# Kernel tuning notes

Hardware: AMD Instinct MI355X
Metric: run time of the kernel (lower is better)

Reference implementation:

```python
import jax, jax.numpy as jnp
import numpy as np

D_MODEL = 1024
N_HEADS = 16
TOP_FACTOR = 5


def setup_inputs() -> dict:
    key = jax.random.key(0)
    ks = jax.random.split(key, 9)
    B, L, D = 2, 4096, D_MODEL
    s = 0.02
    return {
        "x": jax.random.normal(ks[0], (B, L, D), dtype=jnp.float32),
        "Wq": jax.random.normal(ks[1], (D, D), dtype=jnp.float32) * s,
        "bq": jnp.zeros((D,), dtype=jnp.float32),
        "Wk": jax.random.normal(ks[2], (D, D), dtype=jnp.float32) * s,
        "bk": jnp.zeros((D,), dtype=jnp.float32),
        "Wv": jax.random.normal(ks[3], (D, D), dtype=jnp.float32) * s,
        "bv": jnp.zeros((D,), dtype=jnp.float32),
        "Wo": jax.random.normal(ks[4], (D, D), dtype=jnp.float32) * s,
        "bo": jnp.zeros((D,), dtype=jnp.float32),
    }


def reference(x, Wq, bq, Wk, bk, Wv, bv, Wo, bo):
    B, L, D = x.shape
    H = N_HEADS
    hd = D // H
    BH = B * H
    top_u = max(1, L // TOP_FACTOR)

    def proj(W, b):
        # [B,L,D] -> [B*H, L, hd] (matches view + transpose(1,2) in torch)
        y = x @ W.T + b
        return y.reshape(B, L, H, hd).transpose(0, 2, 1, 3).reshape(BH, L, hd)

    Q = proj(Wq, bq)
    K = proj(Wk, bk)
    V = proj(Wv, bv)

    # select top-u queries per (batch,head) by L2 norm
    query_norms = jnp.linalg.norm(Q, axis=2)              # [BH, L]
    _, top_idx = jax.lax.top_k(query_norms, top_u)        # [BH, top_u]
    Q_sel = jnp.take_along_axis(Q, top_idx[:, :, None], axis=1)  # [BH, u, hd]

    scale = 1.0 / (hd ** 0.5)
    scores = jnp.einsum('bud,bld->bul', Q_sel, K) * scale  # [BH, u, L]
    attn = jax.nn.softmax(scores, axis=-1)
    out_sel = jnp.einsum('bul,bld->bud', attn, V)          # [BH, u, hd]

    # scatter selected outputs back; non-selected rows stay zero
    out_full = jnp.zeros((BH, L, hd), dtype=x.dtype)
    out_full = out_full.at[jnp.arange(BH)[:, None], top_idx].set(out_sel)

    out = out_full.reshape(B, H, L, hd).transpose(0, 2, 1, 3).reshape(B, L, D)
    return out @ Wo.T + bo
```

## Files before the change

### kernel.cpp

```cpp
#include <hip/hip_runtime.h>
#include <cstddef>
#include <cstdint>

constexpr int LSEQ = 4096;
constexpr int DM   = 1024;
constexpr int HD   = 64;
constexpr int BHT  = 32;
constexpr int TOPU = 819;
constexpr int MROWS = 8192;

typedef unsigned short u16;
typedef __attribute__((ext_vector_type(8))) short short8v;
typedef __attribute__((ext_vector_type(4))) short short4v;
typedef __attribute__((ext_vector_type(8))) _Float16 half8v;
typedef __attribute__((ext_vector_type(4))) float f32x4;

__device__ __forceinline__ u16 f2bf(float f) {
  uint32_t u = __float_as_uint(f);
  u += 0x7fffu + ((u >> 16) & 1u);
  return (u16)(u >> 16);
}
__device__ __forceinline__ float bf2f(u16 h) {
  return __uint_as_float(((uint32_t)h) << 16);
}

__device__ __forceinline__ void gl16(const void* g, void* l) {
  __builtin_amdgcn_global_load_lds(
      (const __attribute__((address_space(1))) void*)g,
      (__attribute__((address_space(3))) void*)l, 16, 0, 0);
}

__device__ __forceinline__ void inv_swz(int S, int& R, int& C) {
  const int R0 = ((S >> 5) ^ (S >> 7)) & 1;
  const int R1 = (S >> 6) & 1;
  R = ((S >> 6) << 1) | R0;
  C = (((S >> 3) & 1) ^ R0) | ((((S >> 4) & 1) ^ R1) << 1);
}

__device__ __forceinline__ void splitx_body(const float* src, u16* p1, u16* p2,
                                            u16* pb, int i) {
  const float4 a = *reinterpret_cast<const float4*>(src + (size_t)i * 8);
  const float4 b = *reinterpret_cast<const float4*>(src + (size_t)i * 8 + 4);
  float e[8] = {a.x, a.y, a.z, a.w, b.x, b.y, b.z, b.w};
  short8v v1, v2, vb;
  #pragma unroll
  for (int j = 0; j < 8; ++j) {
    _Float16 h1 = (_Float16)e[j];
    float r = e[j] - (float)h1;
    _Float16 h2 = (_Float16)(r * 256.0f);
    v1[j] = __builtin_bit_cast(short, h1);
    v2[j] = __builtin_bit_cast(short, h2);
    vb[j] = (short)f2bf(e[j]);
  }
  *reinterpret_cast<short8v*>(p1 + (size_t)i * 8) = v1;
  *reinterpret_cast<short8v*>(p2 + (size_t)i * 8) = v2;
  *reinterpret_cast<short8v*>(pb + (size_t)i * 8) = vb;
}

__device__ __forceinline__ void split2h_body(const float* src, u16* p1, u16* p2,
                                             int i) {
  const float4 a = *reinterpret_cast<const float4*>(src + (size_t)i * 8);
  const float4 b = *reinterpret_cast<const float4*>(src + (size_t)i * 8 + 4);
  float e[8] = {a.x, a.y, a.z, a.w, b.x, b.y, b.z, b.w};
  short8v v1, v2;
  #pragma unroll
  for (int j = 0; j < 8; ++j) {
    _Float16 h1 = (_Float16)e[j];
    float r = e[j] - (float)h1;
    _Float16 h2 = (_Float16)(r * 256.0f);
    v1[j] = __builtin_bit_cast(short, h1);
    v2[j] = __builtin_bit_cast(short, h2);
  }
  *reinterpret_cast<short8v*>(p1 + (size_t)i * 8) = v1;
  *reinterpret_cast<short8v*>(p2 + (size_t)i * 8) = v2;
}

__device__ __forceinline__ void conv_body(const float* src, u16* dst, int i) {
  const float4 a = *reinterpret_cast<const float4*>(src + (size_t)i * 8);
  const float4 b = *reinterpret_cast<const float4*>(src + (size_t)i * 8 + 4);
  short8v v;
  v[0] = (short)f2bf(a.x); v[1] = (short)f2bf(a.y);
  v[2] = (short)f2bf(a.z); v[3] = (short)f2bf(a.w);
  v[4] = (short)f2bf(b.x); v[5] = (short)f2bf(b.y);
  v[6] = (short)f2bf(b.z); v[7] = (short)f2bf(b.w);
  *reinterpret_cast<short8v*>(dst + (size_t)i * 8) = v;
}

__global__ __launch_bounds__(256) void prep_all(
    const float* __restrict__ x,  const float* __restrict__ Wq,
    const float* __restrict__ Wk, const float* __restrict__ Wv,
    const float* __restrict__ Wo,
    u16* __restrict__ xh1, u16* __restrict__ xh2, u16* __restrict__ x1b,
    u16* __restrict__ wqh1, u16* __restrict__ wqh2,
    u16* __restrict__ Wkb, u16* __restrict__ Wvb, u16* __restrict__ Wob)
{
  const int NX = MROWS * DM / 8;
  const int NW = DM * DM / 8;
  int i = blockIdx.x * 256 + threadIdx.x;
  if (i < NX)  { splitx_body(x, xh1, xh2, x1b, i); return; }
  i -= NX;
  if (i < NW)  { split2h_body(Wq, wqh1, wqh2, i); return; }
  i -= NW;
  if (i < NW)  { conv_body(Wk, Wkb, i); return; }
  i -= NW;
  if (i < NW)  { conv_body(Wv, Wvb, i); return; }
  i -= NW;
  if (i < NW)  { conv_body(Wo, Wob, i); }
}

__global__ __launch_bounds__(256) void gemm_q_split(
    const u16* __restrict__ X1, const u16* __restrict__ X2,
    const u16* __restrict__ W1, const u16* __restrict__ W2,
    const float* __restrict__ bias, float* __restrict__ Y,
    float* __restrict__ norms)
{
  __shared__ u16 As[2][128 * 32];
  __shared__ u16 Bs[2][128 * 32];
  const int tid = threadIdx.x;
  const int m0 = blockIdx.x * 128, n0 = blockIdx.y * 128;
  const int wid = tid >> 6, lane = tid & 63;
  const int wr = (wid >> 1) * 64, wc = (wid & 1) * 64;
  const int c = lane & 15, G = lane >> 4;

  int Rr[2], Cr[2];
  #pragma unroll
  for (int rr = 0; rr < 2; ++rr) inv_swz((tid + rr * 256) * 8, Rr[rr], Cr[rr]);

  f32x4 acc0[4][4], acc1[4][4];
  #pragma unroll
  for (int mt = 0; mt < 4; ++mt)
    #pragma unroll
    for (int nt = 0; nt < 4; ++nt) {
      acc0[mt][nt] = (f32x4){0.f, 0.f, 0.f, 0.f};
      acc1[mt][nt] = (f32x4){0.f, 0.f, 0.f, 0.f};
    }

  for (int k0 = 0; k0 < DM; k0 += 32) {
    #pragma unroll
    for (int rr = 0; rr < 2; ++rr) {
      const size_t goA = (size_t)(m0 + Rr[rr]) * DM + k0 + Cr[rr] * 8;
      const size_t goB = (size_t)(n0 + Rr[rr]) * DM + k0 + Cr[rr] * 8;
      const int lb = wid * 512 + rr * 2048;
      gl16(X1 + goA, &As[0][lb]);
      gl16(X2 + goA, &As[1][lb]);
      gl16(W1 + goB, &Bs[0][lb]);
      gl16(W2 + goB, &Bs[1][lb]);
    }
    __syncthreads();

    half8v bf1[4], bf2[4];
    #pragma unroll
    for (int nt = 0; nt < 4; ++nt) {
      const int n = wc + nt * 16 + c;
      const int eo = (n * 32 + G * 8) ^ ((n & 7) << 3);
      bf1[nt] = *reinterpret_cast<const half8v*>(&Bs[0][eo]);
      bf2[nt] = *reinterpret_cast<const half8v*>(&Bs[1][eo]);
    }
    #pragma unroll
    for (int mt = 0; mt < 4; ++mt) {
      const int m = wr + mt * 16 + c;
      const int eo = (m * 32 + G * 8) ^ ((m & 7) << 3);
      half8v a1 = *reinterpret_cast<const half8v*>(&As[0][eo]);
      half8v a2 = *reinterpret_cast<const half8v*>(&As[1][eo]);
      #pragma unroll
      for (int nt = 0; nt < 4; ++nt) {
        acc0[mt][nt] = __builtin_amdgcn_mfma_f32_16x16x32_f16(a1, bf1[nt], acc0[mt][nt], 0, 0, 0);
        acc1[mt][nt] = __builtin_amdgcn_mfma_f32_16x16x32_f16(a1, bf2[nt], acc1[mt][nt], 0, 0, 0);
        acc1[mt][nt] = __builtin_amdgcn_mfma_f32_16x16x32_f16(a2, bf1[nt], acc1[mt][nt], 0, 0, 0);
      }
    }
    __syncthreads();
  }

  float bb[4];
  #pragma unroll
  for (int nt = 0; nt < 4; ++nt) bb[nt] = bias[n0 + wc + nt * 16 + c];

  float ns[4][4];
  #pragma unroll
  for (int mt = 0; mt < 4; ++mt)
    #pragma unroll
    for (int r = 0; r < 4; ++r) ns[mt][r] = 0.f;

  constexpr float INV256 = 1.0f / 256.0f;
  #pragma unroll
  for (int mt = 0; mt < 4; ++mt) {
    #pragma unroll
    for (int nt = 0; nt < 4; ++nt) {
      const int n = n0 + wc + nt * 16 + c;
      const int h = n >> 6, d = n & 63;
      #pragma unroll
      for (int r = 0; r < 4; ++r) {
        const int m = m0 + wr + mt * 16 + G * 4 + r;
        const int b = m >> 12, l = m & (LSEQ - 1);
        const float val = acc0[mt][nt][r] + acc1[mt][nt][r] * INV256 + bb[nt];
        Y[((size_t)((b << 4) + h) * LSEQ + l) * HD + d] = val;
        ns[mt][r] = fmaf(val, val, ns[mt][r]);
      }
    }
  }
  #pragma unroll
  for (int mt = 0; mt < 4; ++mt)
    #pragma unroll
    for (int r = 0; r < 4; ++r) {
      float v = ns[mt][r];
      v += __shfl_xor(v, 1); v += __shfl_xor(v, 2);
      v += __shfl_xor(v, 4); v += __shfl_xor(v, 8);
      ns[mt][r] = v;
    }
  if (c == 0) {
    const int h = (n0 + wc) >> 6;
    #pragma unroll
    for (int mt = 0; mt < 4; ++mt)
      #pragma unroll
      for (int r = 0; r < 4; ++r) {
        const int m = m0 + wr + mt * 16 + G * 4 + r;
        const int b = m >> 12, l = m & (LSEQ - 1);
        norms[(((size_t)((b << 4) + h)) << 12) + l] = ns[mt][r];
      }
  }
}

__global__ __launch_bounds__(256) void gemm_kv(
    const u16* __restrict__ Xb, const u16* __restrict__ Wkb, const u16* __restrict__ Wvb,
    const float* __restrict__ bkp, const float* __restrict__ bvp,
    u16* __restrict__ Kb, u16* __restrict__ VgT)
{
  __shared__ u16 smem[128 * 136];
  u16* As = smem;
  u16* Bs = smem + 4096;
  const int tid = threadIdx.x;
  const bool isV = blockIdx.y >= 8;
  const int m0 = blockIdx.x * 128, n0 = (blockIdx.y & 7) * 128;
  const u16* Wb = isV ? Wvb : Wkb;
  const float* bias = isV ? bvp : bkp;
  const int wid = tid >> 6, lane = tid & 63;
  const int wr = (wid >> 1) * 64, wc = (wid & 1) * 64;
  const int c = lane & 15, G = lane >> 4;

  int Rr[2], Cr[2];
  #pragma unroll
  for (int rr = 0; rr < 2; ++rr) inv_swz((tid + rr * 256) * 8, Rr[rr], Cr[rr]);

  f32x4 acc[4][4];
  #pragma unroll
  for (int mt = 0; mt < 4; ++mt)
    #pragma unroll
    for (int nt = 0; nt < 4; ++nt)
      acc[mt][nt] = (f32x4){0.f, 0.f, 0.f, 0.f};

  for (int k0 = 0; k0 < DM; k0 += 32) {
    #pragma unroll
    for (int rr = 0; rr < 2; ++rr) {
      const size_t goA = (size_t)(m0 + Rr[rr]) * DM + k0 + Cr[rr] * 8;
      const size_t goB = (size_t)(n0 + Rr[rr]) * DM + k0 + Cr[rr] * 8;
      const int lb = wid * 512 + rr * 2048;
      gl16(Xb + goA, As + lb);
      gl16(Wb + goB, Bs + lb);
    }
    __syncthreads();

    short8v af[4], bf[4];
    #pragma unroll
    for (int mt = 0; mt < 4; ++mt) {
      const int m = wr + mt * 16 + c;
      af[mt] = *reinterpret_cast<const short8v*>(As + ((m * 32 + G * 8) ^ ((m & 7) << 3)));
      const int n = wc + mt * 16 + c;
      bf[mt] = *reinterpret_cast<const short8v*>(Bs + ((n * 32 + G * 8) ^ ((n & 7) << 3)));
    }
    #pragma unroll
    for (int mt = 0; mt < 4; ++mt)
      #pragma unroll
      for (int nt = 0; nt < 4; ++nt)
        acc[mt][nt] = __builtin_amdgcn_mfma_f32_16x16x32_bf16(af[mt], bf[nt], acc[mt][nt], 0, 0, 0);
    __syncthreads();
  }

  float bb[4];
  #pragma unroll
  for (int nt = 0; nt < 4; ++nt) bb[nt] = bias[n0 + wc + nt * 16 + c];

  if (isV) {
    #pragma unroll
    for (int mt = 0; mt < 4; ++mt) {
      #pragma unroll
      for (int nt = 0; nt < 4; ++nt) {
        const int n = wc + nt * 16 + c;
        const int mloc = wr + mt * 16 + G * 4;
        short4v pv;
        #pragma unroll
        for (int r = 0; r < 4; ++r) pv[r] = (short)f2bf(acc[mt][nt][r] + bb[nt]);
        *reinterpret_cast<short4v*>(smem + n * 136 + mloc) = pv;
      }
    }
    __syncthreads();
    const int bb2 = m0 >> 12;
    const int ml0 = m0 & (LSEQ - 1);
    #pragma unroll
    for (int uu = 0; uu < 8; ++uu) {
      const int u = uu * 256 + tid;
      const int n = u >> 4, kg = u & 15;
      short8v vvv = *reinterpret_cast<const short8v*>(smem + n * 136 + kg * 8);
      const int h = (n0 + n) >> 6, d = (n0 + n) & 63;
      *reinterpret_cast<short8v*>(
          VgT + ((size_t)((bb2 << 4) + h) * HD + d) * LSEQ + ml0 + kg * 8) = vvv;
    }
  } else {
    #pragma unroll
    for (int mt = 0; mt < 4; ++mt) {
      #pragma unroll
      for (int nt = 0; nt < 4; ++nt) {
        const int n = n0 + wc + nt * 16 + c;
        const int h = n >> 6, d = n & 63;
        #pragma unroll
        for (int r = 0; r < 4; ++r) {
          const int m = m0 + wr + mt * 16 + G * 4 + r;
          const int b = m >> 12, l = m & (LSEQ - 1);
          Kb[((size_t)((b << 4) + h) * LSEQ + l) * HD + d] = f2bf(acc[mt][nt][r] + bb[nt]);
        }
      }
    }
  }
}

__global__ __launch_bounds__(256) void gemm_out(
    const u16* __restrict__ Xb, const u16* __restrict__ Wb,
    const float* __restrict__ bias, float* __restrict__ Y)
{
  __shared__ u16 As[128 * 32];
  __shared__ u16 Bs[128 * 32];
  const int tid = threadIdx.x;
  const int m0 = blockIdx.x * 128, n0 = blockIdx.y * 128;
  const int wid = tid >> 6, lane = tid & 63;
  const int wr = (wid >> 1) * 64, wc = (wid & 1) * 64;
  const int c = lane & 15, G = lane >> 4;

  int Rr[2], Cr[2];
  #pragma unroll
  for (int rr = 0; rr < 2; ++rr) inv_swz((tid + rr * 256) * 8, Rr[rr], Cr[rr]);

  f32x4 acc[4][4];
  #pragma unroll
  for (int mt = 0; mt < 4; ++mt)
    #pragma unroll
    for (int nt = 0; nt < 4; ++nt)
      acc[mt][nt] = (f32x4){0.f, 0.f, 0.f, 0.f};

  for (int k0 = 0; k0 < DM; k0 += 32) {
    #pragma unroll
    for (int rr = 0; rr < 2; ++rr) {
      const size_t goA = (size_t)(m0 + Rr[rr]) * DM + k0 + Cr[rr] * 8;
      const size_t goB = (size_t)(n0 + Rr[rr]) * DM + k0 + Cr[rr] * 8;
      const int lb = wid * 512 + rr * 2048;
      gl16(Xb + goA, As + lb);
      gl16(Wb + goB, Bs + lb);
    }
    __syncthreads();

    short8v af[4], bf[4];
    #pragma unroll
    for (int mt = 0; mt < 4; ++mt) {
      const int m = wr + mt * 16 + c;
      af[mt] = *reinterpret_cast<const short8v*>(As + ((m * 32 + G * 8) ^ ((m & 7) << 3)));
      const int n = wc + mt * 16 + c;
      bf[mt] = *reinterpret_cast<const short8v*>(Bs + ((n * 32 + G * 8) ^ ((n & 7) << 3)));
    }
    #pragma unroll
    for (int mt = 0; mt < 4; ++mt)
      #pragma unroll
      for (int nt = 0; nt < 4; ++nt)
        acc[mt][nt] = __builtin_amdgcn_mfma_f32_16x16x32_bf16(af[mt], bf[nt], acc[mt][nt], 0, 0, 0);
    __syncthreads();
  }

  float bb[4];
  #pragma unroll
  for (int nt = 0; nt < 4; ++nt) bb[nt] = bias[n0 + wc + nt * 16 + c];

  #pragma unroll
  for (int mt = 0; mt < 4; ++mt) {
    #pragma unroll
    for (int nt = 0; nt < 4; ++nt) {
      const int n = n0 + wc + nt * 16 + c;
      #pragma unroll
      for (int r = 0; r < 4; ++r) {
        const int m = m0 + wr + mt * 16 + G * 4 + r;
        Y[(size_t)m * DM + n] = acc[mt][nt][r] + bb[nt];
      }
    }
  }
}

__global__ __launch_bounds__(1024) void select_topk(
    const float* __restrict__ norms, int* __restrict__ top_idx)
{
  __shared__ unsigned int keys[LSEQ];
  __shared__ unsigned int hist[256];
  __shared__ unsigned int wsums[16];
  __shared__ unsigned int sh_b, sh_above;

  const int tid = threadIdx.x;
  const int bh = blockIdx.x;

  for (int l = tid; l < LSEQ; l += 1024)
    keys[l] = __float_as_uint(norms[bh * LSEQ + l]);
  __syncthreads();

  unsigned int prefix = 0, rem = TOPU, total_gt = 0;
  for (int shift = 24; shift >= 0; shift -= 8) {
    if (tid < 256) hist[tid] = 0;
    __syncthreads();
    for (int l = tid; l < LSEQ; l += 1024) {
      const unsigned int k = keys[l];
      const bool in = (shift == 24) || ((k >> (shift + 8)) == prefix);
      if (in) atomicAdd(&hist[(k >> shift) & 255], 1);
    }
    __syncthreads();
    if (tid == 0) {
      unsigned int cum = 0; int b = 255;
      for (; b > 0; --b) {
        const unsigned int h = hist[b];
        if (cum + h >= rem) break;
        cum += h;
      }
      sh_b = (unsigned int)b; sh_above = cum;
    }
    __syncthreads();
    prefix = (prefix << 8) | sh_b;
    total_gt += sh_above;
    rem -= sh_above;
    __syncthreads();
  }
  const unsigned int T = prefix;

  const int lane = tid & 63, wv = tid >> 6;
  const int l0 = tid * 4;

  {
    unsigned int flags = 0; int cnt = 0;
    #pragma unroll
    for (int j = 0; j < 4; ++j)
      if (keys[l0 + j] > T) { flags |= 1u << j; ++cnt; }
    int incl = cnt;
    #pragma unroll
    for (int off = 1; off < 64; off <<= 1) {
      int nv = __shfl_up(incl, off);
      if (lane >= off) incl += nv;
    }
    if (lane == 63) wsums[wv] = (unsigned int)incl;
    __syncthreads();
    if (tid == 0) {
      unsigned int run = 0;
      for (int w = 0; w < 16; ++w) { unsigned int t = wsums[w]; wsums[w] = run; run += t; }
    }
    __syncthreads();
    unsigned int pos = wsums[wv] + (unsigned int)(incl - cnt);
    #pragma unroll
    for (int j = 0; j < 4; ++j)
      if (flags & (1u << j)) top_idx[bh * TOPU + (pos++)] = l0 + j;
  }
  __syncthreads();

  {
    unsigned int flags = 0; int cnt = 0;
    #pragma unroll
    for (int j = 0; j < 4; ++j)
      if (keys[l0 + j] == T) { flags |= 1u << j; ++cnt; }
    int incl = cnt;
    #pragma unroll
    for (int off = 1; off < 64; off <<= 1) {
      int nv = __shfl_up(incl, off);
      if (lane >= off) incl += nv;
    }
    if (lane == 63) wsums[wv] = (unsigned int)incl;
    __syncthreads();
    if (tid == 0) {
      unsigned int run = 0;
      for (int w = 0; w < 16; ++w) { unsigned int t = wsums[w]; wsums[w] = run; run += t; }
    }
    __syncthreads();
    unsigned int r0 = wsums[wv] + (unsigned int)(incl - cnt);
    #pragma unroll
    for (int j = 0; j < 4; ++j)
      if (flags & (1u << j)) {
        if (r0 < rem) top_idx[bh * TOPU + total_gt + r0] = l0 + j;
        ++r0;
      }
  }
}

__global__ __launch_bounds__(256) void attn_mfma(
    const float* __restrict__ Qf, const u16* __restrict__ Kg,
    const u16* __restrict__ VgT, const int* __restrict__ tix,
    float* __restrict__ Opart, float* __restrict__ MLpart)
{
  __shared__ u16 Kc[128 * 64];
  __shared__ u16 Vt[64 * 128];
  __shared__ u16 Pt[4][16 * 136];

  const int tid = threadIdx.x;
  const int wid = tid >> 6, lane = tid & 63;
  const int c = lane & 15, G = lane >> 4;

  const int l = blockIdx.x;
  const int grp = l >> 3;
  const int bh = (grp / 26) * 8 + (l & 7);
  const int rem = grp % 26;
  const int qb = rem >> 1, ks = rem & 1;

  const size_t bhL = (size_t)bh * LSEQ;
  const int rglob = qb * 64 + wid * 16 + c;
  const int rowidx = (rglob < TOPU) ? tix[bh * TOPU + rglob] : -1;

  short8v qf[2];
  #pragma unroll
  for (int kf = 0; kf < 2; ++kf) {
    if (rowidx >= 0) {
      const float* qp = Qf + (bhL + rowidx) * HD + kf * 32 + G * 8;
      const float4 x0 = *reinterpret_cast<const float4*>(qp);
      const float4 x1 = *reinterpret_cast<const float4*>(qp + 4);
      short8v v;
      v[0] = (short)f2bf(x0.x * 0.125f); v[1] = (short)f2bf(x0.y * 0.125f);
      v[2] = (short)f2bf(x0.z * 0.125f); v[3] = (short)f2bf(x0.w * 0.125f);
      v[4] = (short)f2bf(x1.x * 0.125f); v[5] = (short)f2bf(x1.y * 0.125f);
      v[6] = (short)f2bf(x1.z * 0.125f); v[7] = (short)f2bf(x1.w * 0.125f);
      qf[kf] = v;
    } else {
      short8v v;
      #pragma unroll
      for (int j = 0; j < 8; ++j) v[j] = 0;
      qf[kf] = v;
    }
  }

  float m = -1e30f, lsum = 0.f;
  f32x4 oacc[4];
  #pragma unroll
  for (int dt = 0; dt < 4; ++dt) oacc[dt] = (f32x4){0.f, 0.f, 0.f, 0.f};

  const int ko0 = ks * (LSEQ / 2);
  const int wbase = (tid & ~63) * 8;
  for (int t = 0; t < LSEQ / 256; ++t) {
    const int ko = ko0 + t * 128;
    #pragma unroll
    for (int uu = 0; uu < 4; ++uu) {
      const int S = (uu * 256 + tid) * 8;
      const int key = S >> 6, dgk = ((S >> 3) & 7) ^ (key & 7);
      gl16(Kg + (bhL + ko + key) * HD + dgk * 8, Kc + uu * 2048 + wbase);
      const int d = S >> 7, kgv = ((S >> 3) & 15) ^ (d & 7);
      gl16(VgT + ((size_t)bh * HD + d) * LSEQ + ko + kgv * 8, Vt + uu * 2048 + wbase);
    }
    __syncthreads();

    f32x4 sacc[8];
    __builtin_amdgcn_s_setprio(1);
    #pragma unroll
    for (int kt = 0; kt < 8; ++kt) {
      const int key = kt * 16 + c;
      short8v kb0 = *reinterpret_cast<const short8v*>(
          Kc + key * 64 + (((0 + G) ^ (key & 7)) << 3));
      short8v kb1 = *reinterpret_cast<const short8v*>(
          Kc + key * 64 + (((4 + G) ^ (key & 7)) << 3));
      f32x4 s = (f32x4){0.f, 0.f, 0.f, 0.f};
      s = __builtin_amdgcn_mfma_f32_16x16x32_bf16(kb0, qf[0], s, 0, 0, 0);
      s = __builtin_amdgcn_mfma_f32_16x16x32_bf16(kb1, qf[1], s, 0, 0, 0);
      sacc[kt] = s;
    }
    __builtin_amdgcn_s_setprio(0);

    float smax = -1e30f;
    #pragma unroll
    for (int kt = 0; kt < 8; ++kt) {
      float a0 = fmaxf(sacc[kt][0], sacc[kt][1]);
      float a1 = fmaxf(sacc[kt][2], sacc[kt][3]);
      smax = fmaxf(smax, fmaxf(a0, a1));
    }
    smax = fmaxf(smax, __shfl_xor(smax, 16));
    smax = fmaxf(smax, __shfl_xor(smax, 32));
    const float mnew = fmaxf(m, smax);
    const float corr = __expf(m - mnew);
    float ssum = 0.f;
    #pragma unroll
    for (int kt = 0; kt < 8; ++kt) {
      float p0 = __expf(sacc[kt][0] - mnew);
      float p1 = __expf(sacc[kt][1] - mnew);
      float p2 = __expf(sacc[kt][2] - mnew);
      float p3 = __expf(sacc[kt][3] - mnew);
      ssum += (p0 + p1) + (p2 + p3);
      short4v pv;
      pv[0] = (short)f2bf(p0); pv[1] = (short)f2bf(p1);
      pv[2] = (short)f2bf(p2); pv[3] = (short)f2bf(p3);
      *reinterpret_cast<short4v*>(&Pt[wid][c * 136 + kt * 16 + G * 4]) = pv;
    }
    ssum += __shfl_xor(ssum, 16);
    ssum += __shfl_xor(ssum, 32);
    lsum = lsum * corr + ssum;
    m = mnew;
    #pragma unroll
    for (int dt = 0; dt < 4; ++dt) oacc[dt] *= corr;

    __builtin_amdgcn_s_setprio(1);
    #pragma unroll
    for (int kf = 0; kf < 4; ++kf) {
      short8v pf = *reinterpret_cast<const short8v*>(
          &Pt[wid][c * 136 + kf * 32 + G * 8]);
      #pragma unroll
      for (int dt = 0; dt < 4; ++dt) {
        const int d = dt * 16 + c;
        short8v vf = *reinterpret_cast<const short8v*>(
            Vt + d * 128 + (((kf * 4 + G) ^ (d & 7)) << 3));
        oacc[dt] = __builtin_amdgcn_mfma_f32_16x16x32_bf16(vf, pf, oacc[dt], 0, 0, 0);
      }
    }
    __builtin_amdgcn_s_setprio(0);
    __syncthreads();
  }

  const int q = wid * 16 + c;
  const size_t pb = ((size_t)(bh * 13 + qb) * 2 + ks) * 64 + q;
  float* op = Opart + pb * 64;
  #pragma unroll
  for (int dt = 0; dt < 4; ++dt)
    *reinterpret_cast<f32x4*>(op + dt * 16 + G * 4) = oacc[dt];
  if (G == 0) {
    MLpart[pb * 2]     = m;
    MLpart[pb * 2 + 1] = lsum;
  }
}

__global__ __launch_bounds__(256) void attn_combine(
    const float* __restrict__ Opart, const float* __restrict__ MLpart,
    const int* __restrict__ tix, u16* __restrict__ O1b)
{
  const int bq = blockIdx.x;
  const int bh = bq / 13, qb = bq % 13;
  const int tid = threadIdx.x;
  const int q = tid >> 2, dq = (tid & 3) * 16;
  const int rglob = qb * 64 + q;
  if (rglob >= TOPU) return;
  const int rowidx = tix[bh * TOPU + rglob];

  const size_t p0 = ((size_t)bq * 2 + 0) * 64 + q;
  const size_t p1 = ((size_t)bq * 2 + 1) * 64 + q;
  const float m0 = MLpart[p0 * 2], l0 = MLpart[p0 * 2 + 1];
  const float m1 = MLpart[p1 * 2], l1 = MLpart[p1 * 2 + 1];
  const float mx = fmaxf(m0, m1);
  const float c0 = __expf(m0 - mx), c1 = __expf(m1 - mx);
  const float linv = 1.0f / (l0 * c0 + l1 * c1);

  const int b = bh >> 4, h = bh & 15;
  u16* dst = O1b + (size_t)(b * LSEQ + rowidx) * DM + h * HD + dq;
  const float* o0 = Opart + p0 * 64 + dq;
  const float* o1 = Opart + p1 * 64 + dq;
  #pragma unroll
  for (int i = 0; i < 16; i += 4) {
    float4 a  = *reinterpret_cast<const float4*>(o0 + i);
    float4 bb = *reinterpret_cast<const float4*>(o1 + i);
    short4v o;
    o[0] = (short)f2bf((a.x * c0 + bb.x * c1) * linv);
    o[1] = (short)f2bf((a.y * c0 + bb.y * c1) * linv);
    o[2] = (short)f2bf((a.z * c0 + bb.z * c1) * linv);
    o[3] = (short)f2bf((a.w * c0 + bb.w * c1) * linv);
    *reinterpret_cast<short4v*>(dst + i) = o;
  }
}

extern "C" void kernel_launch(void* const* d_in, const int* in_sizes, int n_in,
                              void* d_out, int out_size, void* d_ws, size_t ws_size,
                              hipStream_t stream) {
  const float* x  = (const float*)d_in[0];
  const float* Wq = (const float*)d_in[1];
  const float* bq = (const float*)d_in[2];
  const float* Wk = (const float*)d_in[3];
  const float* bk = (const float*)d_in[4];
  const float* Wv = (const float*)d_in[5];
  const float* bv = (const float*)d_in[6];
  const float* Wo = (const float*)d_in[7];
  const float* bo = (const float*)d_in[8];
  float* out = (float*)d_out;

  char* w = (char*)d_ws;
  float* Qb = (float*)w;  w += (size_t)BHT * LSEQ * HD * 4;
  u16* xh1  = (u16*)w;    w += (size_t)MROWS * DM * 2;
  u16* xh2  = (u16*)w;    w += (size_t)MROWS * DM * 2;
  u16* x1b  = (u16*)w;    w += (size_t)MROWS * DM * 2;
  u16* VgT  = (u16*)w;    w += (size_t)BHT * HD * LSEQ * 2;
  u16* Wkb  = (u16*)w;    w += (size_t)DM * DM * 2;
  u16* Wvb  = (u16*)w;    w += (size_t)DM * DM * 2;
  u16* Wob  = (u16*)w;    w += (size_t)DM * DM * 2;
  u16* wqh1 = (u16*)w;    w += (size_t)DM * DM * 2;
  u16* wqh2 = (u16*)w;    w += (size_t)DM * DM * 2;
  float* norms = (float*)w; w += (size_t)BHT * LSEQ * 4;

  u16*   O1b  = xh1;
  u16*   Kb   = xh2;
  int*   tix  = (int*)wqh2;
  float* Opart  = (float*)x1b;
  float* MLpart = Opart + (size_t)832 * 64 * 64;

  prep_all<<<6144, 256, 0, stream>>>(x, Wq, Wk, Wv, Wo,
                                     xh1, xh2, x1b, wqh1, wqh2, Wkb, Wvb, Wob);

  gemm_q_split<<<dim3(MROWS / 128, DM / 128), 256, 0, stream>>>(
      xh1, xh2, wqh1, wqh2, bq, Qb, norms);

  gemm_kv<<<dim3(MROWS / 128, 16), 256, 0, stream>>>(x1b, Wkb, Wvb, bk, bv, Kb, VgT);

  select_topk<<<BHT, 1024, 0, stream>>>(norms, tix);

  hipMemsetAsync(O1b, 0, (size_t)MROWS * DM * 2, stream);

  attn_mfma<<<832, 256, 0, stream>>>(Qb, Kb, VgT, tix, Opart, MLpart);
  attn_combine<<<416, 256, 0, stream>>>(Opart, MLpart, tix, O1b);

  gemm_out<<<dim3(MROWS / 128, DM / 128), 256, 0, stream>>>(O1b, Wob, bo, out);
}
```

Before: 310.0 us.

## Fuse Q/K/V projections into one launch and split attention keys into four segments

```diff
diff --git a/kernel.cpp b/kernel.cpp
--- a/kernel.cpp
+++ b/kernel.cpp
@@ -8,6 +8,7 @@
 constexpr int BHT  = 32;
 constexpr int TOPU = 819;
 constexpr int MROWS = 8192;
+constexpr int NSEG = 4;
 
 typedef unsigned short u16;
 typedef __attribute__((ext_vector_type(8))) short short8v;
@@ -108,16 +109,19 @@
   if (i < NW)  { conv_body(Wo, Wob, i); }
 }
 
-__global__ __launch_bounds__(256) void gemm_q_split(
+__device__ __forceinline__ void proj_q_body(
+    u16* smem,
     const u16* __restrict__ X1, const u16* __restrict__ X2,
     const u16* __restrict__ W1, const u16* __restrict__ W2,
     const float* __restrict__ bias, float* __restrict__ Y,
-    float* __restrict__ norms)
+    float* __restrict__ norms, int bx, int ny)
 {
-  __shared__ u16 As[2][128 * 32];
-  __shared__ u16 Bs[2][128 * 32];
+  u16* As1 = smem;
+  u16* As2 = smem + 4096;
+  u16* Bs1 = smem + 8192;
+  u16* Bs2 = smem + 12288;
   const int tid = threadIdx.x;
-  const int m0 = blockIdx.x * 128, n0 = blockIdx.y * 128;
+  const int m0 = bx * 128, n0 = ny * 128;
   const int wid = tid >> 6, lane = tid & 63;
   const int wr = (wid >> 1) * 64, wc = (wid & 1) * 64;
   const int c = lane & 15, G = lane >> 4;
@@ -141,10 +145,10 @@
       const size_t goA = (size_t)(m0 + Rr[rr]) * DM + k0 + Cr[rr] * 8;
       const size_t goB = (size_t)(n0 + Rr[rr]) * DM + k0 + Cr[rr] * 8;
       const int lb = wid * 512 + rr * 2048;
-      gl16(X1 + goA, &As[0][lb]);
-      gl16(X2 + goA, &As[1][lb]);
-      gl16(W1 + goB, &Bs[0][lb]);
-      gl16(W2 + goB, &Bs[1][lb]);
+      gl16(X1 + goA, As1 + lb);
+      gl16(X2 + goA, As2 + lb);
+      gl16(W1 + goB, Bs1 + lb);
+      gl16(W2 + goB, Bs2 + lb);
     }
     __syncthreads();
 
@@ -153,15 +157,15 @@
     for (int nt = 0; nt < 4; ++nt) {
       const int n = wc + nt * 16 + c;
       const int eo = (n * 32 + G * 8) ^ ((n & 7) << 3);
-      bf1[nt] = *reinterpret_cast<const half8v*>(&Bs[0][eo]);
-      bf2[nt] = *reinterpret_cast<const half8v*>(&Bs[1][eo]);
+      bf1[nt] = *reinterpret_cast<const half8v*>(Bs1 + eo);
+      bf2[nt] = *reinterpret_cast<const half8v*>(Bs2 + eo);
     }
     #pragma unroll
     for (int mt = 0; mt < 4; ++mt) {
       const int m = wr + mt * 16 + c;
       const int eo = (m * 32 + G * 8) ^ ((m & 7) << 3);
-      half8v a1 = *reinterpret_cast<const half8v*>(&As[0][eo]);
-      half8v a2 = *reinterpret_cast<const half8v*>(&As[1][eo]);
+      half8v a1 = *reinterpret_cast<const half8v*>(As1 + eo);
+      half8v a2 = *reinterpret_cast<const half8v*>(As2 + eo);
       #pragma unroll
       for (int nt = 0; nt < 4; ++nt) {
         acc0[mt][nt] = __builtin_amdgcn_mfma_f32_16x16x32_f16(a1, bf1[nt], acc0[mt][nt], 0, 0, 0);
@@ -221,19 +225,15 @@
   }
 }
 
-__global__ __launch_bounds__(256) void gemm_kv(
-    const u16* __restrict__ Xb, const u16* __restrict__ Wkb, const u16* __restrict__ Wvb,
-    const float* __restrict__ bkp, const float* __restrict__ bvp,
-    u16* __restrict__ Kb, u16* __restrict__ VgT)
+__device__ __forceinline__ void proj_kv_body(
+    u16* smem, const u16* __restrict__ Xb, const u16* __restrict__ Wb,
+    const float* __restrict__ bias, u16* __restrict__ Kb, u16* __restrict__ VgT,
+    bool isV, int bx, int ny)
 {
-  __shared__ u16 smem[128 * 136];
   u16* As = smem;
   u16* Bs = smem + 4096;
   const int tid = threadIdx.x;
-  const bool isV = blockIdx.y >= 8;
-  const int m0 = blockIdx.x * 128, n0 = (blockIdx.y & 7) * 128;
-  const u16* Wb = isV ? Wvb : Wkb;
-  const float* bias = isV ? bvp : bkp;
+  const int m0 = bx * 128, n0 = ny * 128;
   const int wid = tid >> 6, lane = tid & 63;
   const int wr = (wid >> 1) * 64, wc = (wid & 1) * 64;
   const int c = lane & 15, G = lane >> 4;
@@ -320,6 +320,26 @@
         }
       }
     }
+  }
+}
+
+__global__ __launch_bounds__(256) void gemm_proj(
+    const u16* __restrict__ X1, const u16* __restrict__ X2, const u16* __restrict__ Xb,
+    const u16* __restrict__ W1, const u16* __restrict__ W2,
+    const u16* __restrict__ Wkb, const u16* __restrict__ Wvb,
+    const float* __restrict__ bq, const float* __restrict__ bk, const float* __restrict__ bv,
+    float* __restrict__ Qb, float* __restrict__ norms,
+    u16* __restrict__ Kb, u16* __restrict__ VgT, int y_off)
+{
+  __shared__ __align__(16) u16 smem[17408];
+  const int by = blockIdx.y + y_off;
+  const int bx = blockIdx.x;
+  if (by < 8) {
+    proj_q_body(smem, X1, X2, W1, W2, bq, Qb, norms, bx, by);
+  } else if (by < 16) {
+    proj_kv_body(smem, Xb, Wvb, bv, Kb, VgT, true, bx, by - 8);
+  } else {
+    proj_kv_body(smem, Xb, Wkb, bk, Kb, VgT, false, bx, by - 16);
   }
 }
 
@@ -492,7 +512,7 @@
 __global__ __launch_bounds__(256) void attn_mfma(
     const float* __restrict__ Qf, const u16* __restrict__ Kg,
     const u16* __restrict__ VgT, const int* __restrict__ tix,
-    float* __restrict__ Opart, float* __restrict__ MLpart)
+    u16* __restrict__ OpartB, float* __restrict__ MLpart)
 {
   __shared__ u16 Kc[128 * 64];
   __shared__ u16 Vt[64 * 128];
@@ -504,9 +524,9 @@
 
   const int l = blockIdx.x;
   const int grp = l >> 3;
-  const int bh = (grp / 26) * 8 + (l & 7);
-  const int rem = grp % 26;
-  const int qb = rem >> 1, ks = rem & 1;
+  const int bh = (grp / 52) * 8 + (l & 7);
+  const int rem = grp % 52;
+  const int qb = rem >> 2, ks = rem & 3;
 
   const size_t bhL = (size_t)bh * LSEQ;
   const int rglob = qb * 64 + wid * 16 + c;
@@ -538,9 +558,9 @@
   #pragma unroll
   for (int dt = 0; dt < 4; ++dt) oacc[dt] = (f32x4){0.f, 0.f, 0.f, 0.f};
 
-  const int ko0 = ks * (LSEQ / 2);
+  const int ko0 = ks * (LSEQ / NSEG);
   const int wbase = (tid & ~63) * 8;
-  for (int t = 0; t < LSEQ / 256; ++t) {
+  for (int t = 0; t < LSEQ / NSEG / 128; ++t) {
     const int ko = ko0 + t * 128;
     #pragma unroll
     for (int uu = 0; uu < 4; ++uu) {
@@ -617,11 +637,15 @@
   }
 
   const int q = wid * 16 + c;
-  const size_t pb = ((size_t)(bh * 13 + qb) * 2 + ks) * 64 + q;
-  float* op = Opart + pb * 64;
-  #pragma unroll
-  for (int dt = 0; dt < 4; ++dt)
-    *reinterpret_cast<f32x4*>(op + dt * 16 + G * 4) = oacc[dt];
+  const size_t pb = ((size_t)((bh * 13 + qb) * NSEG + ks)) * 64 + q;
+  u16* op = OpartB + pb * 64;
+  #pragma unroll
+  for (int dt = 0; dt < 4; ++dt) {
+    short4v o;
+    o[0] = (short)f2bf(oacc[dt][0]); o[1] = (short)f2bf(oacc[dt][1]);
+    o[2] = (short)f2bf(oacc[dt][2]); o[3] = (short)f2bf(oacc[dt][3]);
+    *reinterpret_cast<short4v*>(op + dt * 16 + G * 4) = o;
+  }
   if (G == 0) {
     MLpart[pb * 2]     = m;
     MLpart[pb * 2 + 1] = lsum;
@@ -629,7 +653,7 @@
 }
 
 __global__ __launch_bounds__(256) void attn_combine(
-    const float* __restrict__ Opart, const float* __restrict__ MLpart,
+    const u16* __restrict__ OpartB, const float* __restrict__ MLpart,
     const int* __restrict__ tix, u16* __restrict__ O1b)
 {
   const int bq = blockIdx.x;
@@ -640,28 +664,38 @@
   if (rglob >= TOPU) return;
   const int rowidx = tix[bh * TOPU + rglob];
 
-  const size_t p0 = ((size_t)bq * 2 + 0) * 64 + q;
-  const size_t p1 = ((size_t)bq * 2 + 1) * 64 + q;
-  const float m0 = MLpart[p0 * 2], l0 = MLpart[p0 * 2 + 1];
-  const float m1 = MLpart[p1 * 2], l1 = MLpart[p1 * 2 + 1];
-  const float mx = fmaxf(m0, m1);
-  const float c0 = __expf(m0 - mx), c1 = __expf(m1 - mx);
-  const float linv = 1.0f / (l0 * c0 + l1 * c1);
+  size_t p[NSEG];
+  float mi[NSEG], li[NSEG];
+  #pragma unroll
+  for (int i = 0; i < NSEG; ++i) {
+    p[i] = ((size_t)bq * NSEG + i) * 64 + q;
+    mi[i] = MLpart[p[i] * 2];
+    li[i] = MLpart[p[i] * 2 + 1];
+  }
+  float mx = fmaxf(fmaxf(mi[0], mi[1]), fmaxf(mi[2], mi[3]));
+  float ci[NSEG], lsum = 0.f;
+  #pragma unroll
+  for (int i = 0; i < NSEG; ++i) { ci[i] = __expf(mi[i] - mx); lsum += li[i] * ci[i]; }
+  const float linv = 1.0f / lsum;
+
+  float acc[16];
+  #pragma unroll
+  for (int j = 0; j < 16; ++j) acc[j] = 0.f;
+  #pragma unroll
+  for (int i = 0; i < NSEG; ++i) {
+    const u16* src = OpartB + p[i] * 64 + dq;
+    #pragma unroll
+    for (int j = 0; j < 16; ++j) acc[j] += bf2f(src[j]) * ci[i];
+  }
 
   const int b = bh >> 4, h = bh & 15;
   u16* dst = O1b + (size_t)(b * LSEQ + rowidx) * DM + h * HD + dq;
-  const float* o0 = Opart + p0 * 64 + dq;
-  const float* o1 = Opart + p1 * 64 + dq;
-  #pragma unroll
-  for (int i = 0; i < 16; i += 4) {
-    float4 a  = *reinterpret_cast<const float4*>(o0 + i);
-    float4 bb = *reinterpret_cast<const float4*>(o1 + i);
+  #pragma unroll
+  for (int j0 = 0; j0 < 16; j0 += 4) {
     short4v o;
-    o[0] = (short)f2bf((a.x * c0 + bb.x * c1) * linv);
-    o[1] = (short)f2bf((a.y * c0 + bb.y * c1) * linv);
-    o[2] = (short)f2bf((a.z * c0 + bb.z * c1) * linv);
-    o[3] = (short)f2bf((a.w * c0 + bb.w * c1) * linv);
-    *reinterpret_cast<short4v*>(dst + i) = o;
+    #pragma unroll
+    for (int j = 0; j < 4; ++j) o[j] = (short)f2bf(acc[j0 + j] * linv);
+    *reinterpret_cast<short4v*>(dst + j0) = o;
   }
 }
 
@@ -691,27 +725,35 @@
   u16* wqh1 = (u16*)w;    w += (size_t)DM * DM * 2;
   u16* wqh2 = (u16*)w;    w += (size_t)DM * DM * 2;
   float* norms = (float*)w; w += (size_t)BHT * LSEQ * 4;
-
-  u16*   O1b  = xh1;
-  u16*   Kb   = xh2;
-  int*   tix  = (int*)wqh2;
-  float* Opart  = (float*)x1b;
-  float* MLpart = Opart + (size_t)832 * 64 * 64;
+  u16* Kb_ext = (u16*)w;  w += (size_t)BHT * LSEQ * HD * 2;
+
+  const bool fusedK = ws_size >= (size_t)(w - (char*)d_ws);
+  u16* Kb       = fusedK ? Kb_ext : xh2;
+  u16* OpartB   = fusedK ? xh2 : x1b;
+  const int NPB = BHT * 13 * NSEG * 64;
+  float* MLpart = (float*)(OpartB + (size_t)NPB * 64);
+  u16*   O1b    = xh1;
+  int*   tix    = (int*)wqh2;
 
   prep_all<<<6144, 256, 0, stream>>>(x, Wq, Wk, Wv, Wo,
                                      xh1, xh2, x1b, wqh1, wqh2, Wkb, Wvb, Wob);
 
-  gemm_q_split<<<dim3(MROWS / 128, DM / 128), 256, 0, stream>>>(
-      xh1, xh2, wqh1, wqh2, bq, Qb, norms);
-
-  gemm_kv<<<dim3(MROWS / 128, 16), 256, 0, stream>>>(x1b, Wkb, Wvb, bk, bv, Kb, VgT);
+  if (fusedK) {
+    gemm_proj<<<dim3(64, 24), 256, 0, stream>>>(
+        xh1, xh2, x1b, wqh1, wqh2, Wkb, Wvb, bq, bk, bv, Qb, norms, Kb, VgT, 0);
+  } else {
+    gemm_proj<<<dim3(64, 16), 256, 0, stream>>>(
+        xh1, xh2, x1b, wqh1, wqh2, Wkb, Wvb, bq, bk, bv, Qb, norms, Kb, VgT, 0);
+    gemm_proj<<<dim3(64, 8), 256, 0, stream>>>(
+        xh1, xh2, x1b, wqh1, wqh2, Wkb, Wvb, bq, bk, bv, Qb, norms, Kb, VgT, 16);
+  }
 
   select_topk<<<BHT, 1024, 0, stream>>>(norms, tix);
 
   hipMemsetAsync(O1b, 0, (size_t)MROWS * DM * 2, stream);
 
-  attn_mfma<<<832, 256, 0, stream>>>(Qb, Kb, VgT, tix, Opart, MLpart);
-  attn_combine<<<416, 256, 0, stream>>>(Opart, MLpart, tix, O1b);
+  attn_mfma<<<BHT * 13 * NSEG, 256, 0, stream>>>(Qb, Kb, VgT, tix, OpartB, MLpart);
+  attn_combine<<<BHT * 13, 256, 0, stream>>>(OpartB, MLpart, tix, O1b);
 
   gemm_out<<<dim3(MROWS / 128, DM / 128), 256, 0, stream>>>(O1b, Wob, bo, out);
 }
```

Measured after the change: 325.6 us. 1.05x slower.
